# Kernel optimization log

Hardware: AMD Instinct MI355X
Metric: run time of the kernel (lower is better)

The kernel has to match this reference:

```python
import jax, jax.numpy as jnp
import numpy as np

THRESHOLD = 0.3
EPS = 1e-8  # matches torch F.cosine_similarity eps


def _normalize(x):
    # L2-normalize rows with torch-style eps clamp on the norm
    n = jnp.sqrt(jnp.sum(x * x, axis=-1, keepdims=True))
    return x / jnp.maximum(n, EPS)


def _triu_cos_self(x):
    # pairwise cosine similarity of x with itself, upper triangle (offset=1)
    xn = _normalize(x)
    csm = xn @ xn.T  # [N, N]
    i, j = jnp.triu_indices(x.shape[0], k=1)
    return csm[i, j]


def setup_inputs() -> dict:
    key = jax.random.key(0)
    k1, k2 = jax.random.split(key)
    stereos = jax.random.normal(k1, (96, 768), dtype=jnp.float32)
    astereos = jax.random.normal(k2, (96, 768), dtype=jnp.float32)
    return {"stereos": stereos, "astereos": astereos}


def reference(stereos, astereos):
    # positive sims: triu of each self cosine-similarity matrix, concatenated
    pos_sim = jnp.concatenate(
        [_triu_cos_self(stereos), _triu_cos_self(astereos)], axis=0
    )  # [P]
    # negative sims: full cross cosine similarity, flattened
    neg = _normalize(astereos) @ _normalize(stereos).T  # [M, N]
    neg_sim = neg.reshape(-1)  # [Q]
    # hinge over the full pos x neg outer product: mean(max(0, neg - pos + thr))
    diff = neg_sim[None, :] - pos_sim[:, None] + THRESHOLD  # [P, Q]
    return jnp.mean(jnp.maximum(diff, 0.0))
```

## Files before the change

### kernel.cpp

```cpp
#include <hip/hip_runtime.h>
#include <math.h>

#define NROWS   96
#define DIM     768
#define THRESH  0.3f
#define NPAIR   4560
#define PTOT    9120
#define QTOT    9216
#define NBLK    576
#define NWAVES  (NBLK * 4)
#define SPR     24
#define NGRP    24
#define GRPSZ   24

#define AST(p, v) __hip_atomic_store((p), (v), __ATOMIC_RELAXED, __HIP_MEMORY_SCOPE_AGENT)
#define ALD(p)    __hip_atomic_load((p), __ATOMIC_RELAXED, __HIP_MEMORY_SCOPE_AGENT)


__device__ __forceinline__ float d12(
    const float4& x0, const float4& x1, const float4& x2,
    const float4& y0, const float4& y1, const float4& y2)
{
    return x0.x*y0.x + x0.y*y0.y + x0.z*y0.z + x0.w*y0.w
         + x1.x*y1.x + x1.y*y1.y + x1.z*y1.z + x1.w*y1.w
         + x2.x*y2.x + x2.y*y2.y + x2.z*y2.z + x2.w*y2.w;
}

template <int N>
__device__ __forceinline__ void wreduce(float* v)
{
#pragma unroll
    for (int off = 32; off; off >>= 1) {
#pragma unroll
        for (int k = 0; k < N; k++) v[k] += __shfl_down(v[k], off);
    }
}

__global__ __launch_bounds__(256) void fused_kernel(
    const float* __restrict__ stereos, const float* __restrict__ astereos,
    float* __restrict__ pos, float* __restrict__ neg,
    float* __restrict__ slotSp, float* __restrict__ slotSn,
    float* __restrict__ slotMx, float* __restrict__ slotMn,
    unsigned int* __restrict__ gctr0, unsigned int* __restrict__ sctr,
    const unsigned int* __restrict__ ref, size_t gstride,
    float* __restrict__ out)
{
    __shared__ float  sSp[4], sSn[4], sMx[4], sMn[4];
    __shared__ int    sLast;
    __shared__ double rsp[4], rsn[4], redd[4];
    __shared__ float  rmx[4], rmn[4];
    __shared__ double bcd[2];
    __shared__ float  bnmin;
    __shared__ int    rare;
    __shared__ float  sNeg[QTOT];

    int tid  = threadIdx.x;
    int wave = tid >> 6, lane = tid & 63;

    unsigned int base = 0;
    if (tid == 0) base = ALD(ref);

    int gw = blockIdx.x * 4 + wave;
    int i  = gw / SPR;
    int j0 = (gw - i * SPR) * 4;

    float acc[13];
    {
        const float4* aS = (const float4*)(stereos  + i * DIM);
        const float4* aC = (const float4*)(astereos + i * DIM);
        float4 as0 = aS[lane], as1 = aS[lane + 64], as2 = aS[lane + 128];
        float4 ac0 = aC[lane], ac1 = aC[lane + 64], ac2 = aC[lane + 128];
        acc[0] = d12(as0, as1, as2, as0, as1, as2);
        acc[1] = d12(ac0, ac1, ac2, ac0, ac1, ac2);
#pragma unroll
        for (int m = 0; m < 4; m++) {
            const float4* b = (const float4*)(stereos + (j0 + m) * DIM);
            float4 b0 = b[lane], b1 = b[lane + 64], b2 = b[lane + 128];
            acc[2 + m]  = d12(b0, b1, b2, b0, b1, b2);
            acc[6 + m]  = d12(as0, as1, as2, b0, b1, b2);
            acc[10 + m] = d12(ac0, ac1, ac2, b0, b1, b2);
        }
        wreduce<13>(acc);
    }
    int sw = NWAVES - 1 - gw;
    int ia = sw / SPR, ja0 = (sw - ia * SPR) * 4;
    float accA[9];
    {
        const float4* aA = (const float4*)(astereos + ia * DIM);
        float4 a0 = aA[lane], a1 = aA[lane + 64], a2 = aA[lane + 128];
        accA[0] = d12(a0, a1, a2, a0, a1, a2);
#pragma unroll
        for (int m = 0; m < 4; m++) {
            const float4* b = (const float4*)(astereos + (ja0 + m) * DIM);
            float4 b0 = b[lane], b1 = b[lane + 64], b2 = b[lane + 128];
            accA[1 + m] = d12(b0, b1, b2, b0, b1, b2);
            accA[5 + m] = d12(a0, a1, a2, b0, b1, b2);
        }
        wreduce<9>(accA);
    }

    if (lane == 0) {
        float wsp = 0.f, wsn = 0.f, wmx = -INFINITY, wmn = INFINITY;
        float invaS = 1.0f / fmaxf(sqrtf(acc[0]), 1e-8f);
        float invaC = 1.0f / fmaxf(sqrtf(acc[1]), 1e-8f);
        int baseS = (i * (191 - i)) / 2 - i - 1;
#pragma unroll
        for (int m = 0; m < 4; m++) {
            float invb = 1.0f / fmaxf(sqrtf(acc[2 + m]), 1e-8f);
            float sc = acc[10 + m] * invaC * invb;
            AST(&neg[i * NROWS + j0 + m], sc);
            wsn += sc; wmn = fminf(wmn, sc);
            if (j0 + m > i) {
                float ss = acc[6 + m] * invaS * invb;
                AST(&pos[baseS + j0 + m], ss);
                wsp += ss; wmx = fmaxf(wmx, ss);
            }
        }
        float invaA = 1.0f / fmaxf(sqrtf(accA[0]), 1e-8f);
        int baseA = (ia * (191 - ia)) / 2 - ia - 1;
#pragma unroll
        for (int m = 0; m < 4; m++) {
            if (ja0 + m > ia) {
                float invb = 1.0f / fmaxf(sqrtf(accA[1 + m]), 1e-8f);
                float sa = accA[5 + m] * invaA * invb;
                AST(&pos[NPAIR + baseA + ja0 + m], sa);
                wsp += sa; wmx = fmaxf(wmx, sa);
            }
        }
        sSp[wave] = wsp; sSn[wave] = wsn; sMx[wave] = wmx; sMn[wave] = wmn;
    }
    __syncthreads();

    if (tid == 0) {
        AST(&slotSp[blockIdx.x], sSp[0] + sSp[1] + sSp[2] + sSp[3]);
        AST(&slotSn[blockIdx.x], sSn[0] + sSn[1] + sSn[2] + sSn[3]);
        AST(&slotMx[blockIdx.x], fmaxf(fmaxf(sMx[0], sMx[1]), fmaxf(sMx[2], sMx[3])));
        AST(&slotMn[blockIdx.x], fminf(fminf(sMn[0], sMn[1]), fminf(sMn[2], sMn[3])));
        asm volatile("s_waitcnt vmcnt(0)" ::: "memory");
        int g = blockIdx.x / GRPSZ;
        unsigned int* gctr = (unsigned int*)((char*)gctr0 + (size_t)g * gstride);
        unsigned int old = atomicAdd(gctr, 1u);
        int win = 0;
        if (((old - base) % (unsigned)GRPSZ) == (unsigned)(GRPSZ - 1)) {
            unsigned int old2 = atomicAdd(sctr, 1u);
            win = (((old2 - base) % (unsigned)NGRP) == (unsigned)(NGRP - 1));
        }
        sLast = win;
    }
    __syncthreads();
    if (!sLast) return;

    double sp = 0.0, sn = 0.0;
    float mx = -INFINITY, mn = INFINITY;
    for (int f = tid; f < NBLK; f += 256) {
        sp += (double)ALD(&slotSp[f]);
        sn += (double)ALD(&slotSn[f]);
        mx = fmaxf(mx, ALD(&slotMx[f]));
        mn = fminf(mn, ALD(&slotMn[f]));
    }
    for (int off = 32; off; off >>= 1) {
        sp += __shfl_down(sp, off);
        sn += __shfl_down(sn, off);
        mx = fmaxf(mx, __shfl_down(mx, off));
        mn = fminf(mn, __shfl_down(mn, off));
    }
    if (lane == 0) { rsp[wave] = sp; rsn[wave] = sn;
                     rmx[wave] = mx; rmn[wave] = mn; }
    __syncthreads();
    if (tid == 0) {
        bcd[0] = rsp[0] + rsp[1] + rsp[2] + rsp[3];
        bcd[1] = rsn[0] + rsn[1] + rsn[2] + rsn[3];
        float pm = fmaxf(fmaxf(rmx[0], rmx[1]), fmaxf(rmx[2], rmx[3]));
        float nm = fminf(fminf(rmn[0], rmn[1]), fminf(rmn[2], rmn[3]));
        bnmin = nm;
        rare = (pm - nm > THRESH) ? 1 : 0;
    }
    __syncthreads();

    double corr = 0.0;
    if (rare) {
        for (int q = tid; q < QTOT; q += 256) sNeg[q] = ALD(&neg[q]);
        __syncthreads();
        float nmv = bnmin;
        for (int p = tid; p < PTOT; p += 256) {
            float pv = ALD(&pos[p]);
            if (pv - nmv > THRESH) {
                for (int q = 0; q < QTOT; q++) {
                    float d = pv - THRESH - sNeg[q];
                    if (d > 0.f) corr += (double)d;
                }
            }
        }
    }
    for (int off = 32; off; off >>= 1) corr += __shfl_down(corr, off);
    if (lane == 0) redd[wave] = corr;
    __syncthreads();
    if (tid == 0) {
        corr = redd[0] + redd[1] + redd[2] + redd[3];
        double PQ = (double)PTOT * (double)QTOT;
        double total = (double)PTOT * bcd[1] - (double)QTOT * bcd[0]
                     + PQ * (double)THRESH + corr;
        out[0] = (float)(total / PQ);
    }
}

extern "C" void kernel_launch(void* const* d_in, const int* in_sizes, int n_in,
                              void* d_out, int out_size, void* d_ws, size_t ws_size,
                              hipStream_t stream)
{
    const float* stereos  = (const float*)d_in[0];
    const float* astereos = (const float*)d_in[1];

    char* ws = (char*)d_ws;
    float* pos    = (float*)ws;
    float* neg    = (float*)(ws + 36480);
    float* slotSp = (float*)(ws + 73344);
    float* slotSn = (float*)(ws + 75648);
    float* slotMx = (float*)(ws + 77952);
    float* slotMn = (float*)(ws + 80256);

    size_t gctr_off, gstride, sctr_off, ref_off;
    if (ws_size >= (1u << 19) + 4) {
        gctr_off = (size_t)1 << 18;
        gstride  = 4096;
        sctr_off = (size_t)3 << 17;
        ref_off  = (size_t)1 << 19;
    } else {
        gctr_off = 82688;
        gstride  = 0;
        sctr_off = 82816;
        ref_off  = 82944;
    }
    unsigned int* gctr0 = (unsigned int*)(ws + gctr_off);
    unsigned int* sctr  = (unsigned int*)(ws + sctr_off);
    const unsigned int* ref = (const unsigned int*)(ws + ref_off);

    fused_kernel<<<NBLK, 256, 0, stream>>>(stereos, astereos, pos, neg,
                                           slotSp, slotSn, slotMx, slotMn,
                                           gctr0, sctr, ref, gstride,
                                           (float*)d_out);
}
```

Before: 59.96 us.

## Split astereos self-similarity into dedicated blocks covering only upper-triangle tiles

Each wave used to compute both the stereos/cross tile and a mirrored astereos tile, including lower-triangle tiles whose results were thrown away. The astereos pairs now get their own 300 blocks that enumerate only tiles touching the upper triangle. The stereos/cross blocks drop that extra work, so the launch grows to 876 shorter blocks. The group counters are adjusted for a partial last group with a fixed counter stride. That fixed stride may overrun the small-workspace fallback layout.

```diff
diff --git a/kernel.cpp b/kernel.cpp
--- a/kernel.cpp
+++ b/kernel.cpp
@@ -1,17 +1,18 @@
 #include <hip/hip_runtime.h>
 #include <math.h>
 
-#define NROWS   96
-#define DIM     768
-#define THRESH  0.3f
-#define NPAIR   4560
-#define PTOT    9120
-#define QTOT    9216
-#define NBLK    576
-#define NWAVES  (NBLK * 4)
-#define SPR     24
-#define NGRP    24
-#define GRPSZ   24
+#define NROWS    96
+#define DIM      768
+#define THRESH   0.3f
+#define NPAIR    4560
+#define PTOT     9120
+#define QTOT     9216
+#define SPR      24
+#define NBLK_SC  576
+#define NBLK_A   300
+#define NBLK_TOT 876
+#define GRPSZ    24
+#define NGRP     37
 
 #define AST(p, v) __hip_atomic_store((p), (v), __ATOMIC_RELAXED, __HIP_MEMORY_SCOPE_AGENT)
 #define ALD(p)    __hip_atomic_load((p), __ATOMIC_RELAXED, __HIP_MEMORY_SCOPE_AGENT)
@@ -42,8 +43,7 @@
     float* __restrict__ slotSp, float* __restrict__ slotSn,
     float* __restrict__ slotMx, float* __restrict__ slotMn,
     unsigned int* __restrict__ gctr0, unsigned int* __restrict__ sctr,
-    const unsigned int* __restrict__ ref, size_t gstride,
-    float* __restrict__ out)
+    const unsigned int* __restrict__ ref, float* __restrict__ out)
 {
     __shared__ float  sSp[4], sSn[4], sMx[4], sMn[4];
     __shared__ int    sLast;
@@ -60,75 +60,87 @@
     unsigned int base = 0;
     if (tid == 0) base = ALD(ref);
 
-    int gw = blockIdx.x * 4 + wave;
-    int i  = gw / SPR;
-    int j0 = (gw - i * SPR) * 4;
-
-    float acc[13];
-    {
-        const float4* aS = (const float4*)(stereos  + i * DIM);
-        const float4* aC = (const float4*)(astereos + i * DIM);
-        float4 as0 = aS[lane], as1 = aS[lane + 64], as2 = aS[lane + 128];
-        float4 ac0 = aC[lane], ac1 = aC[lane + 64], ac2 = aC[lane + 128];
-        acc[0] = d12(as0, as1, as2, as0, as1, as2);
-        acc[1] = d12(ac0, ac1, ac2, ac0, ac1, ac2);
-#pragma unroll
-        for (int m = 0; m < 4; m++) {
-            const float4* b = (const float4*)(stereos + (j0 + m) * DIM);
-            float4 b0 = b[lane], b1 = b[lane + 64], b2 = b[lane + 128];
-            acc[2 + m]  = d12(b0, b1, b2, b0, b1, b2);
-            acc[6 + m]  = d12(as0, as1, as2, b0, b1, b2);
-            acc[10 + m] = d12(ac0, ac1, ac2, b0, b1, b2);
-        }
-        wreduce<13>(acc);
-    }
-    int sw = NWAVES - 1 - gw;
-    int ia = sw / SPR, ja0 = (sw - ia * SPR) * 4;
-    float accA[9];
-    {
-        const float4* aA = (const float4*)(astereos + ia * DIM);
-        float4 a0 = aA[lane], a1 = aA[lane + 64], a2 = aA[lane + 128];
-        accA[0] = d12(a0, a1, a2, a0, a1, a2);
-#pragma unroll
-        for (int m = 0; m < 4; m++) {
-            const float4* b = (const float4*)(astereos + (ja0 + m) * DIM);
-            float4 b0 = b[lane], b1 = b[lane + 64], b2 = b[lane + 128];
-            accA[1 + m] = d12(b0, b1, b2, b0, b1, b2);
-            accA[5 + m] = d12(a0, a1, a2, b0, b1, b2);
-        }
-        wreduce<9>(accA);
-    }
-
-    if (lane == 0) {
-        float wsp = 0.f, wsn = 0.f, wmx = -INFINITY, wmn = INFINITY;
-        float invaS = 1.0f / fmaxf(sqrtf(acc[0]), 1e-8f);
-        float invaC = 1.0f / fmaxf(sqrtf(acc[1]), 1e-8f);
-        int baseS = (i * (191 - i)) / 2 - i - 1;
-#pragma unroll
-        for (int m = 0; m < 4; m++) {
-            float invb = 1.0f / fmaxf(sqrtf(acc[2 + m]), 1e-8f);
-            float sc = acc[10 + m] * invaC * invb;
-            AST(&neg[i * NROWS + j0 + m], sc);
-            wsn += sc; wmn = fminf(wmn, sc);
-            if (j0 + m > i) {
-                float ss = acc[6 + m] * invaS * invb;
-                AST(&pos[baseS + j0 + m], ss);
-                wsp += ss; wmx = fmaxf(wmx, ss);
-            }
-        }
-        float invaA = 1.0f / fmaxf(sqrtf(accA[0]), 1e-8f);
-        int baseA = (ia * (191 - ia)) / 2 - ia - 1;
-#pragma unroll
-        for (int m = 0; m < 4; m++) {
-            if (ja0 + m > ia) {
-                float invb = 1.0f / fmaxf(sqrtf(accA[1 + m]), 1e-8f);
-                float sa = accA[5 + m] * invaA * invb;
-                AST(&pos[NPAIR + baseA + ja0 + m], sa);
-                wsp += sa; wmx = fmaxf(wmx, sa);
-            }
-        }
-        sSp[wave] = wsp; sSn[wave] = wsn; sMx[wave] = wmx; sMn[wave] = wmn;
-    }
+    float wsp = 0.f, wsn = 0.f, wmx = -INFINITY, wmn = INFINITY;
+
+    if (blockIdx.x < NBLK_SC) {
+        int gw = blockIdx.x * 4 + wave;
+        int i  = gw / SPR;
+        int j0 = (gw - i * SPR) * 4;
+        float acc[13];
+        {
+            const float4* aS = (const float4*)(stereos  + i * DIM);
+            const float4* aC = (const float4*)(astereos + i * DIM);
+            float4 as0 = aS[lane], as1 = aS[lane + 64], as2 = aS[lane + 128];
+            float4 ac0 = aC[lane], ac1 = aC[lane + 64], ac2 = aC[lane + 128];
+            acc[0] = d12(as0, as1, as2, as0, as1, as2);
+            acc[1] = d12(ac0, ac1, ac2, ac0, ac1, ac2);
+#pragma unroll
+            for (int m = 0; m < 4; m++) {
+                const float4* b = (const float4*)(stereos + (j0 + m) * DIM);
+                float4 b0 = b[lane], b1 = b[lane + 64], b2 = b[lane + 128];
+                acc[2 + m]  = d12(b0, b1, b2, b0, b1, b2);
+                acc[6 + m]  = d12(as0, as1, as2, b0, b1, b2);
+                acc[10 + m] = d12(ac0, ac1, ac2, b0, b1, b2);
+            }
+            wreduce<13>(acc);
+        }
+        if (lane == 0) {
+            float invaS = 1.0f / fmaxf(sqrtf(acc[0]), 1e-8f);
+            float invaC = 1.0f / fmaxf(sqrtf(acc[1]), 1e-8f);
+            int baseS = (i * (191 - i)) / 2 - i - 1;
+#pragma unroll
+            for (int m = 0; m < 4; m++) {
+                float invb = 1.0f / fmaxf(sqrtf(acc[2 + m]), 1e-8f);
+                float sc = acc[10 + m] * invaC * invb;
+                AST(&neg[i * NROWS + j0 + m], sc);
+                wsn += sc; wmn = fminf(wmn, sc);
+                if (j0 + m > i) {
+                    float ss = acc[6 + m] * invaS * invb;
+                    AST(&pos[baseS + j0 + m], ss);
+                    wsp += ss; wmx = fmaxf(wmx, ss);
+                }
+            }
+        }
+    } else {
+        int aw = (blockIdx.x - NBLK_SC) * 4 + wave;
+        int s = 0;
+        {
+            int r = aw;
+            while (r >= 4 * s + 4) { r -= 4 * s + 4; s++; }
+            aw = r;
+        }
+        int ia = aw, ja0 = 4 * s;
+        float accA[9];
+        {
+            const float4* aA = (const float4*)(astereos + ia * DIM);
+            float4 a0 = aA[lane], a1 = aA[lane + 64], a2 = aA[lane + 128];
+            accA[0] = d12(a0, a1, a2, a0, a1, a2);
+#pragma unroll
+            for (int m = 0; m < 4; m++) {
+                const float4* b = (const float4*)(astereos + (ja0 + m) * DIM);
+                float4 b0 = b[lane], b1 = b[lane + 64], b2 = b[lane + 128];
+                accA[1 + m] = d12(b0, b1, b2, b0, b1, b2);
+                accA[5 + m] = d12(a0, a1, a2, b0, b1, b2);
+            }
+            wreduce<9>(accA);
+        }
+        if (lane == 0) {
+            float invaA = 1.0f / fmaxf(sqrtf(accA[0]), 1e-8f);
+            int baseA = (ia * (191 - ia)) / 2 - ia - 1;
+#pragma unroll
+            for (int m = 0; m < 4; m++) {
+                if (ja0 + m > ia) {
+                    float invb = 1.0f / fmaxf(sqrtf(accA[1 + m]), 1e-8f);
+                    float sa = accA[5 + m] * invaA * invb;
+                    AST(&pos[NPAIR + baseA + ja0 + m], sa);
+                    wsp += sa; wmx = fmaxf(wmx, sa);
+                }
+            }
+        }
+    }
+
+    if (lane == 0) { sSp[wave] = wsp; sSn[wave] = wsn;
+                     sMx[wave] = wmx; sMn[wave] = wmn; }
     __syncthreads();
 
     if (tid == 0) {
@@ -138,10 +150,11 @@
         AST(&slotMn[blockIdx.x], fminf(fminf(sMn[0], sMn[1]), fminf(sMn[2], sMn[3])));
         asm volatile("s_waitcnt vmcnt(0)" ::: "memory");
         int g = blockIdx.x / GRPSZ;
-        unsigned int* gctr = (unsigned int*)((char*)gctr0 + (size_t)g * gstride);
+        unsigned int cnt = (unsigned int)min(GRPSZ, NBLK_TOT - g * GRPSZ);
+        unsigned int* gctr = (unsigned int*)((char*)gctr0 + (size_t)g * 2048);
         unsigned int old = atomicAdd(gctr, 1u);
         int win = 0;
-        if (((old - base) % (unsigned)GRPSZ) == (unsigned)(GRPSZ - 1)) {
+        if (((old - base) % cnt) == cnt - 1u) {
             unsigned int old2 = atomicAdd(sctr, 1u);
             win = (((old2 - base) % (unsigned)NGRP) == (unsigned)(NGRP - 1));
         }
@@ -152,7 +165,7 @@
 
     double sp = 0.0, sn = 0.0;
     float mx = -INFINITY, mn = INFINITY;
-    for (int f = tid; f < NBLK; f += 256) {
+    for (int f = tid; f < NBLK_TOT; f += 256) {
         sp += (double)ALD(&slotSp[f]);
         sn += (double)ALD(&slotSn[f]);
         mx = fmaxf(mx, ALD(&slotMx[f]));
@@ -215,28 +228,25 @@
     float* pos    = (float*)ws;
     float* neg    = (float*)(ws + 36480);
     float* slotSp = (float*)(ws + 73344);
-    float* slotSn = (float*)(ws + 75648);
-    float* slotMx = (float*)(ws + 77952);
-    float* slotMn = (float*)(ws + 80256);
-
-    size_t gctr_off, gstride, sctr_off, ref_off;
+    float* slotSn = (float*)(ws + 77440);
+    float* slotMx = (float*)(ws + 81536);
+    float* slotMn = (float*)(ws + 85632);
+
+    size_t gctr_off, sctr_off, ref_off;
     if (ws_size >= (1u << 19) + 4) {
         gctr_off = (size_t)1 << 18;
-        gstride  = 4096;
-        sctr_off = (size_t)3 << 17;
+        sctr_off = (size_t)7 << 16;
         ref_off  = (size_t)1 << 19;
     } else {
-        gctr_off = 82688;
-        gstride  = 0;
-        sctr_off = 82816;
-        ref_off  = 82944;
+        gctr_off = 89856;
+        sctr_off = 89984;
+        ref_off  = 90112;
     }
     unsigned int* gctr0 = (unsigned int*)(ws + gctr_off);
     unsigned int* sctr  = (unsigned int*)(ws + sctr_off);
     const unsigned int* ref = (const unsigned int*)(ws + ref_off);
 
-    fused_kernel<<<NBLK, 256, 0, stream>>>(stereos, astereos, pos, neg,
-                                           slotSp, slotSn, slotMx, slotMn,
-                                           gctr0, sctr, ref, gstride,
-                                           (float*)d_out);
-}
+    fused_kernel<<<NBLK_TOT, 256, 0, stream>>>(stereos, astereos, pos, neg,
+                                               slotSp, slotSn, slotMx, slotMn,
+                                               gctr0, sctr, ref, (float*)d_out);
+}
```

Measured after the change: 60.22 us. No clear change (+0.4%).
